# Kernel optimization log

Hardware: AMD Instinct MI355X
Metric: run time of the kernel (lower is better)

The kernel has to match this reference:

```python
import jax, jax.numpy as jnp
import numpy as np
import math

B, S, D, H = 2, 2048, 4096, 32
HD = D // H  # 128


def setup_inputs() -> dict:
    key = jax.random.key(0)
    ks = jax.random.split(key, 8)
    x = jax.random.normal(ks[0], (B, S, D), dtype=jnp.float32)
    wq = jax.random.normal(ks[1], (D, D), dtype=jnp.float32) * 0.02
    wk = jax.random.normal(ks[2], (D, D), dtype=jnp.float32) * 0.02
    wv = jax.random.normal(ks[3], (D, D), dtype=jnp.float32) * 0.02
    wo = jax.random.normal(ks[4], (D, D), dtype=jnp.float32) * 0.02
    # RoPE frequencies as in LLaMA: theta = 10000^{-2i/hd}
    inv_freq = 1.0 / (10000.0 ** (np.arange(0, HD, 2, dtype=np.float32) / HD))  # [HD/2]
    t = np.arange(S, dtype=np.float32)
    freqs = np.outer(t, inv_freq)  # [S, HD/2]
    freqs_cos = jnp.asarray(np.cos(freqs))
    freqs_sin = jnp.asarray(np.sin(freqs))
    # additive causal mask [1,1,S,S]
    neg = jnp.full((S, S), -1e9, dtype=jnp.float32)
    mask = jnp.triu(neg, k=1)[None, None, :, :]
    return {"x": x, "wq": wq, "wk": wk, "wv": wv, "wo": wo,
            "freqs_cos": freqs_cos, "freqs_sin": freqs_sin, "mask": mask}


def _apply_rope(t, cos, sin):
    # t: [b, s, h, hd]; cos/sin: [s, hd/2]. Complex mult on (even, odd) pairs.
    tr = t.reshape(*t.shape[:-1], HD // 2, 2)
    xr, xi = tr[..., 0], tr[..., 1]
    c = cos[None, :, None, :]
    s = sin[None, :, None, :]
    out_r = xr * c - xi * s
    out_i = xr * s + xi * c
    return jnp.stack([out_r, out_i], axis=-1).reshape(t.shape)


def reference(x, wq, wk, wv, wo, freqs_cos, freqs_sin, mask):
    b, s, d = x.shape
    # projections (nn.Linear: y = x @ W^T)
    xq = (x @ wq.T).reshape(b, s, H, HD)
    xk = (x @ wk.T).reshape(b, s, H, HD)
    xv = (x @ wv.T).reshape(b, s, H, HD)
    xq = _apply_rope(xq, freqs_cos, freqs_sin)
    xk = _apply_rope(xk, freqs_cos, freqs_sin)
    # [b,h,q,k] scores, softmax in fp32, then attend
    scores = jnp.einsum('bqhd,bkhd->bhqk', xq, xk) / math.sqrt(HD)
    scores = scores + mask
    probs = jax.nn.softmax(scores.astype(jnp.float32), axis=-1).astype(xq.dtype)
    out = jnp.einsum('bhqk,bkhd->bqhd', probs, xv).reshape(b, s, d)
    return out @ wo.T
```

## Files before the change

kernel.cpp:

```cpp
#include <hip/hip_runtime.h>

typedef __bf16 bf16x8 __attribute__((ext_vector_type(8)));
typedef float f32x4 __attribute__((ext_vector_type(4)));
typedef float f32x16 __attribute__((ext_vector_type(16)));
typedef unsigned short u16;
typedef unsigned int u32;
typedef u16 u16x8 __attribute__((ext_vector_type(8)));
typedef u16 u16x4 __attribute__((ext_vector_type(4)));
typedef u32 u32x4 __attribute__((ext_vector_type(4)));

#define B_ 2
#define S_ 2048
#define D_ 4096
#define H_ 32
#define HD_ 128
#define SM_SCALE 0.08838834764831845f
#define C2_ 0.12751743f

__device__ __forceinline__ u16 f2bf(float f) {
  __bf16 h = (__bf16)f;
  return __builtin_bit_cast(unsigned short, h);
}
__device__ __forceinline__ float bf2f(u16 u) {
  return (float)__builtin_bit_cast(__bf16, u);
}

#define GLD_TO_LDS16(gsrc, ldst)                                                     \
  __builtin_amdgcn_global_load_lds((__attribute__((address_space(1))) void*)(gsrc),  \
                                   (__attribute__((address_space(3))) void*)(ldst),  \
                                   16, 0, 0)

__global__ __launch_bounds__(256) void cvt5_kernel(const float* __restrict__ s0,
                                                   const float* __restrict__ s1,
                                                   const float* __restrict__ s2,
                                                   const float* __restrict__ s3,
                                                   const float* __restrict__ s4,
                                                   u16* __restrict__ d0,
                                                   u16* __restrict__ d1,
                                                   u16* __restrict__ d2,
                                                   u16* __restrict__ d3,
                                                   u16* __restrict__ d4,
                                                   int n4) {
  const int region = blockIdx.x >> 9;
  const float* src = region == 0 ? s0 : region == 1 ? s1 : region == 2 ? s2
                   : region == 3 ? s3 : s4;
  u16* dst = region == 0 ? d0 : region == 1 ? d1 : region == 2 ? d2
           : region == 3 ? d3 : d4;
  int i = (blockIdx.x & 511) * 256 + threadIdx.x;
  const int stride = 512 * 256;
  for (; i < n4; i += stride) {
    float4 v = reinterpret_cast<const float4*>(src)[i];
    u16x4 o;
    o[0] = f2bf(v.x); o[1] = f2bf(v.y); o[2] = f2bf(v.z); o[3] = f2bf(v.w);
    reinterpret_cast<u16x4*>(dst)[i] = o;
  }
}


#define LGKM0()                                            \
  do {                                                     \
    asm volatile("s_waitcnt lgkmcnt(0)" ::: "memory");     \
    __builtin_amdgcn_sched_barrier(0);                     \
  } while (0)

__device__ __forceinline__ void fill_af(bf16x8 (&dst)[4], const u16* half_base,
                                        int wr, int lane, int ks) {
#pragma unroll
  for (int m = 0; m < 4; ++m) {
    int rr = wr * 64 + m * 16 + (lane & 15);
    int c8 = (ks * 4 + (lane >> 4)) ^ (rr & 7);
    dst[m] = *reinterpret_cast<const bf16x8*>(half_base + rr * 64 + c8 * 8);
  }
}
__device__ __forceinline__ void fill_bf(bf16x8 (&dst)[2][2], const u16* half_base,
                                        int wn, int lane) {
#pragma unroll
  for (int ks = 0; ks < 2; ++ks)
#pragma unroll
    for (int n = 0; n < 2; ++n) {
      int rr = wn * 32 + n * 16 + (lane & 15);
      int c8 = (ks * 4 + (lane >> 4)) ^ (rr & 7);
      dst[ks][n] = *reinterpret_cast<const bf16x8*>(half_base + rr * 64 + c8 * 8);
    }
}

#define MFMA8(MQ, NQ, KS, AF, BF)                                                \
  do {                                                                           \
    __builtin_amdgcn_s_setprio(1);                                               \
    _Pragma("unroll") for (int m = 0; m < 4; ++m)                                \
      _Pragma("unroll") for (int n = 0; n < 2; ++n)                              \
        acc[(MQ) * 4 + m][(NQ) * 2 + n] =                                        \
            __builtin_amdgcn_mfma_f32_16x16x32_bf16(                             \
                (AF)[m], (BF)[KS][n], acc[(MQ) * 4 + m][(NQ) * 2 + n], 0, 0, 0); \
    __builtin_amdgcn_s_setprio(0);                                               \
  } while (0)

template <typename OutT, bool ROPE>
__global__ __launch_bounds__(512, 2) void gemm256_kernel(const u16* __restrict__ A,
                                                         const u16* __restrict__ Bw,
                                                         OutT* __restrict__ C,
                                                         int M, int N, int K,
                                                         const float* __restrict__ fc,
                                                         const float* __restrict__ fs) {
  __shared__ u16 As[2][2][8192];
  __shared__ u16 Bs[2][2][8192];
  const int tid = threadIdx.x;
  const int lane = tid & 63;
  const int w = tid >> 6;
  const int wr = w >> 2;
  const int wn = w & 3;
  const int nbx = N >> 8;
  const int nby = M >> 8;
  const int nwg = nby * nbx;
  int tr, tc;
  if (nby == 16 && nbx == 16) {
    int xcd = blockIdx.x & 7, j = blockIdx.x >> 3;
    tr = (xcd >> 1) * 4 + (j >> 3);
    tc = (xcd & 1) * 8 + (j & 7);
  } else {
    int wg = blockIdx.x;
    if ((nwg & 7) == 0) wg = (wg & 7) * (nwg >> 3) + (wg >> 3);
    tr = wg / nbx; tc = wg % nbx;
  }

  const size_t arow0 = (size_t)tr * 256;
  const size_t brow0 = (size_t)tc * 256;
  const int KT = K >> 6;

  auto stageA = [&](int t, int half) {
    if (t >= KT) return;
    const int k0 = t << 6;
    u16* base = &As[t & 1][half][0];
#pragma unroll
    for (int i = 0; i < 2; ++i) {
      int q = i * 512 + tid;
      int r = q >> 3;
      int c8 = (q & 7) ^ (r & 7);
      GLD_TO_LDS16(A + (arow0 + half * 128 + r) * K + k0 + c8 * 8, base + q * 8);
    }
  };
  auto stageB = [&](int t, int half) {
    if (t >= KT) return;
    const int k0 = t << 6;
    u16* base = &Bs[t & 1][half][0];
#pragma unroll
    for (int i = 0; i < 2; ++i) {
      int q = i * 512 + tid;
      int r = q >> 3;
      int c8 = (q & 7) ^ (r & 7);
      GLD_TO_LDS16(Bw + (brow0 + half * 128 + r) * K + k0 + c8 * 8, base + q * 8);
    }
  };

  f32x4 acc[8][4] = {};
  bf16x8 afX[4], afY[4], bf0[2][2], bf1[2][2];

  stageA(0, 0); stageA(0, 1); stageB(0, 0); stageB(0, 1);
  stageB(1, 0); stageB(1, 1); stageA(1, 1);
  asm volatile("s_waitcnt vmcnt(4)" ::: "memory");
  __builtin_amdgcn_s_barrier();
  __builtin_amdgcn_sched_barrier(0);
  fill_af(afX, &As[0][0][0], wr, lane, 0);
  fill_bf(bf0, &Bs[0][0][0], wn, lane);

  for (int k = 0; k < KT; ++k) {
    const int buf = k & 1, nb = buf ^ 1;
    const u16* A0 = &As[buf][0][0];
    const u16* A1 = &As[buf][1][0];
    const u16* B1L = &Bs[buf][1][0];
    const u16* A0n = &As[nb][0][0];
    const u16* B0n = &Bs[nb][0][0];

    LGKM0();
    fill_af(afY, A0, wr, lane, 1);
    fill_bf(bf1, B1L, wn, lane);
    stageA(k + 1, 0);
    MFMA8(0, 0, 0, afX, bf0);
    LGKM0();
    fill_af(afX, A1, wr, lane, 0);
    MFMA8(0, 0, 1, afY, bf0);
    __builtin_amdgcn_s_barrier();

    LGKM0();
    fill_af(afY, A1, wr, lane, 1);
    stageB(k + 2, 0);
    MFMA8(1, 0, 0, afX, bf0);
    LGKM0();
    fill_af(afX, A1, wr, lane, 0);
    MFMA8(1, 0, 1, afY, bf0);
    __builtin_amdgcn_s_barrier();

    LGKM0();
    fill_af(afY, A1, wr, lane, 1);
    stageB(k + 2, 1);
    MFMA8(1, 1, 0, afX, bf1);
    LGKM0();
    fill_af(afX, A0, wr, lane, 0);
    MFMA8(1, 1, 1, afY, bf1);
    __builtin_amdgcn_s_barrier();

    LGKM0();
    fill_af(afY, A0, wr, lane, 1);
    MFMA8(0, 1, 0, afX, bf1);
    LGKM0();
    stageA(k + 2, 1);
    if (k >= KT - 3) asm volatile("s_waitcnt vmcnt(0)" ::: "memory");
    else             asm volatile("s_waitcnt vmcnt(4)" ::: "memory");
    __builtin_amdgcn_s_barrier();
    __builtin_amdgcn_sched_barrier(0);
    if (k + 1 < KT) {
      fill_af(afX, A0n, wr, lane, 0);
      fill_bf(bf0, B0n, wn, lane);
    }
    MFMA8(0, 1, 1, afY, bf1);
    __builtin_amdgcn_s_barrier();
  }

#pragma unroll
  for (int mi = 0; mi < 8; ++mi) {
    const int mq = mi >> 2, m = mi & 3;
#pragma unroll
    for (int ni = 0; ni < 4; ++ni) {
      const int nq = ni >> 1, n = ni & 1;
#pragma unroll
      for (int r = 0; r < 4; ++r) {
        size_t row = arow0 + mq * 128 + wr * 64 + m * 16 + ((lane >> 4) << 2) + r;
        size_t col = (size_t)tc * 256 + nq * 128 + wn * 32 + n * 16 + (lane & 15);
        float v = acc[mi][ni][r];
        if constexpr (ROPE) {
          float o = __shfl_xor(v, 1);
          int s = (int)(row & (S_ - 1));
          int p = (wn * 32 + n * 16 + (lane & 14)) >> 1;
          float cv = fc[(s << 6) + p];
          float sv = fs[(s << 6) + p];
          v = (lane & 1) ? (v * cv + o * sv) : (v * cv - o * sv);
        }
        if constexpr (__is_same(OutT, float)) {
          C[row * N + col] = v;
        } else {
          C[row * N + col] = f2bf(v);
        }
      }
    }
  }
}

__global__ __launch_bounds__(512, 2) void attn_kernel(const u16* __restrict__ Q,
                                                      const u16* __restrict__ K,
                                                      const u16* __restrict__ V,
                                                      u16* __restrict__ O) {
  __shared__ u16 Ks[2][64 * 128];
  __shared__ u16 Vt[2][128 * 64];

  const int blk = blockIdx.x;
  const int pr = blk >> 6;
  const int bh = blk & 63;
  const int b = bh >> 5, h = bh & 31;
  const int tid = threadIdx.x, lane = tid & 63, w = tid >> 6;
  const int l31 = lane & 31;
  const int hi = lane >> 5;
  const int r0 = lane >> 1;
  const int dc = 2 * w + (lane & 1);
  const int vd0 = dc * 8;

  for (int ph = 0; ph < 2; ++ph) {
    const int qt = ph == 0 ? 7 - pr : pr;
    const int q0 = qt << 8;
    const int wq0 = q0 + w * 32;
    const int qg = wq0 + l31;

    bf16x8 qf[8];
#pragma unroll
    for (int kb = 0; kb < 8; ++kb)
      qf[kb] = *reinterpret_cast<const bf16x8*>(Q + (size_t)(b * S_ + qg) * D_ + h * HD_ + kb * 16 + hi * 8);

    f32x16 oacc[4] = {};
    float mrun = -__builtin_inff(), lrun = 0.f;

    const int ntiles = 4 * qt + 4;
    u16x8 vr0, vr1;

    {
#pragma unroll
      for (int it = 0; it < 2; ++it) {
        int ff = it * 512 + tid;
        int row = ff >> 4, cc = ff & 15;
        int scc = cc ^ (row & 7);
        GLD_TO_LDS16(K + (size_t)(b * S_ + row) * D_ + h * HD_ + scc * 8, &Ks[0][ff << 3]);
      }
      vr0 = *reinterpret_cast<const u16x8*>(V + (size_t)(b * S_ + 2 * r0) * D_ + h * HD_ + vd0);
      vr1 = *reinterpret_cast<const u16x8*>(V + (size_t)(b * S_ + 2 * r0 + 1) * D_ + h * HD_ + vd0);
      u32* vt32 = reinterpret_cast<u32*>(&Vt[0][0]);
#pragma unroll
      for (int j = 0; j < 8; ++j) {
        int d = vd0 + j;
        u32 val = (u32)vr0[j] | ((u32)vr1[j] << 16);
        vt32[d * 32 + ((r0 >> 2) ^ j) * 4 + (r0 & 3)] = val;
      }
    }
    __syncthreads();

    for (int t = 0; t < ntiles; ++t) {
      const int cur = t & 1, nxt = cur ^ 1;
      const bool pre = (t + 1 < ntiles);
      if (pre) {
        const int kv1 = (t + 1) << 6;
#pragma unroll
        for (int it = 0; it < 2; ++it) {
          int ff = it * 512 + tid;
          int row = ff >> 4, cc = ff & 15;
          int scc = cc ^ (row & 7);
          GLD_TO_LDS16(K + (size_t)(b * S_ + kv1 + row) * D_ + h * HD_ + scc * 8, &Ks[nxt][ff << 3]);
        }
        vr0 = *reinterpret_cast<const u16x8*>(V + (size_t)(b * S_ + kv1 + 2 * r0) * D_ + h * HD_ + vd0);
        vr1 = *reinterpret_cast<const u16x8*>(V + (size_t)(b * S_ + kv1 + 2 * r0 + 1) * D_ + h * HD_ + vd0);
      }

      const int kv0 = t << 6;
      if (kv0 <= wq0 + 31) {
        f32x16 st[2] = {};
        __builtin_amdgcn_s_setprio(1);
#pragma unroll
        for (int kvh = 0; kvh < 2; ++kvh) {
#pragma unroll
          for (int kb = 0; kb < 8; ++kb) {
            int row = kvh * 32 + l31;
            int cc = (2 * kb + hi) ^ (row & 7);
            bf16x8 kf = *reinterpret_cast<const bf16x8*>(&Ks[cur][(row << 7) + (cc << 3)]);
            st[kvh] = __builtin_amdgcn_mfma_f32_32x32x16_bf16(kf, qf[kb], st[kvh], 0, 0, 0);
          }
        }
        __builtin_amdgcn_s_setprio(0);

        if (kv0 + 63 > wq0) {
#pragma unroll
          for (int kvh = 0; kvh < 2; ++kvh)
#pragma unroll
            for (int r = 0; r < 16; ++r) {
              int kvg = kv0 + kvh * 32 + (r & 3) + 8 * (r >> 2) + 4 * hi;
              if (kvg > qg) st[kvh][r] = -1e30f;
            }
        }

        float vmax = -1e30f;
#pragma unroll
        for (int kvh = 0; kvh < 2; ++kvh)
#pragma unroll
          for (int r = 0; r < 16; ++r) vmax = fmaxf(vmax, st[kvh][r]);
        vmax = fmaxf(vmax, __shfl_xor(vmax, 32));
        if (!__all(vmax <= mrun + 64.0f)) {
          float mnew = fmaxf(mrun, vmax);
          float sc = exp2f((mrun - mnew) * C2_);
          mrun = mnew;
          lrun *= sc;
#pragma unroll
          for (int db = 0; db < 4; ++db)
#pragma unroll
            for (int r = 0; r < 16; ++r) oacc[db][r] *= sc;
        }
        float psum = 0.f;
#pragma unroll
        for (int kvh = 0; kvh < 2; ++kvh)
#pragma unroll
          for (int r = 0; r < 16; ++r) {
            float p = exp2f((st[kvh][r] - mrun) * C2_);
            st[kvh][r] = p;
            psum += p;
          }
        psum += __shfl_xor(psum, 32);
        lrun += psum;

        __builtin_amdgcn_s_setprio(1);
#pragma unroll
        for (int h2 = 0; h2 < 2; ++h2)
#pragma unroll
          for (int s2 = 0; s2 < 2; ++s2) {
            const int rb = s2 * 8;
            u32 w0, w1, w2, w3;
            asm("v_cvt_pk_bf16_f32 %0, %1, %2" : "=v"(w0) : "v"(st[h2][rb + 0]), "v"(st[h2][rb + 1]));
            asm("v_cvt_pk_bf16_f32 %0, %1, %2" : "=v"(w1) : "v"(st[h2][rb + 2]), "v"(st[h2][rb + 3]));
            asm("v_cvt_pk_bf16_f32 %0, %1, %2" : "=v"(w2) : "v"(st[h2][rb + 4]), "v"(st[h2][rb + 5]));
            asm("v_cvt_pk_bf16_f32 %0, %1, %2" : "=v"(w3) : "v"(st[h2][rb + 6]), "v"(st[h2][rb + 7]));
            u32 sw0 = (u32)__shfl_xor((int)w0, 32);
            u32 sw1 = (u32)__shfl_xor((int)w1, 32);
            u32 sw2 = (u32)__shfl_xor((int)w2, 32);
            u32 sw3 = (u32)__shfl_xor((int)w3, 32);
            u32x4 fw;
            fw[0] = hi ? sw2 : w0;
            fw[1] = hi ? sw3 : w1;
            fw[2] = hi ? w2 : sw0;
            fw[3] = hi ? w3 : sw1;
            bf16x8 pfrag = __builtin_bit_cast(bf16x8, fw);
#pragma unroll
            for (int db = 0; db < 4; ++db) {
              int d = db * 32 + l31;
              int cc = (h2 * 4 + s2 * 2 + hi) ^ (d & 7);
              bf16x8 va = *reinterpret_cast<const bf16x8*>(&Vt[cur][(d << 6) + (cc << 3)]);
              oacc[db] = __builtin_amdgcn_mfma_f32_32x32x16_bf16(va, pfrag, oacc[db], 0, 0, 0);
            }
          }
        __builtin_amdgcn_s_setprio(0);
      }

      if (pre) {
        u32* vt32 = reinterpret_cast<u32*>(&Vt[nxt][0]);
#pragma unroll
        for (int j = 0; j < 8; ++j) {
          int d = vd0 + j;
          u32 val = (u32)vr0[j] | ((u32)vr1[j] << 16);
          vt32[d * 32 + ((r0 >> 2) ^ j) * 4 + (r0 & 3)] = val;
        }
      }
      __syncthreads();
    }

    const float rinv = 1.0f / lrun;
#pragma unroll
    for (int db = 0; db < 4; ++db)
#pragma unroll
      for (int g = 0; g < 4; ++g) {
        u16x4 o4;
#pragma unroll
        for (int j = 0; j < 4; ++j) o4[j] = f2bf(oacc[db][g * 4 + j] * rinv);
        int d = db * 32 + g * 8 + 4 * hi;
        *reinterpret_cast<u16x4*>(O + (size_t)(b * S_ + qg) * D_ + h * HD_ + d) = o4;
      }
  }
}

extern "C" void kernel_launch(void* const* d_in, const int* in_sizes, int n_in,
                              void* d_out, int out_size, void* d_ws, size_t ws_size,
                              hipStream_t stream) {
  const float* x = (const float*)d_in[0];
  const float* wq = (const float*)d_in[1];
  const float* wk = (const float*)d_in[2];
  const float* wv = (const float*)d_in[3];
  const float* wo = (const float*)d_in[4];
  const float* fc = (const float*)d_in[5];
  const float* fs = (const float*)d_in[6];
  float* out = (float*)d_out;

  const size_t SLOT = (size_t)B_ * S_ * D_;
  u16* ws = (u16*)d_ws;
  u16* wqb = ws + 0 * SLOT;
  u16* wkb = ws + 1 * SLOT;
  u16* wvb = ws + 2 * SLOT;
  u16* wob = ws + 3 * SLOT;
  u16* xb  = ws + 4 * SLOT;
  u16* Qb  = ws + 5 * SLOT;
  u16* Kb  = ws + 6 * SLOT;
  u16* Vb  = ws + 7 * SLOT;
  u16* Ob  = xb;

  const int n4 = (int)(SLOT / 4);
  cvt5_kernel<<<2560, 256, 0, stream>>>(x, wq, wk, wv, wo, xb, wqb, wkb, wvb, wob, n4);

  gemm256_kernel<u16, true><<<256, 512, 0, stream>>>(xb, wqb, Qb, B_ * S_, D_, D_, fc, fs);
  gemm256_kernel<u16, true><<<256, 512, 0, stream>>>(xb, wkb, Kb, B_ * S_, D_, D_, fc, fs);
  gemm256_kernel<u16, false><<<256, 512, 0, stream>>>(xb, wvb, Vb, B_ * S_, D_, D_, fc, fs);

  attn_kernel<<<256, 512, 0, stream>>>(Qb, Kb, Vb, Ob);

  gemm256_kernel<float, false><<<256, 512, 0, stream>>>(Ob, wob, out, B_ * S_, D_, D_, fc, fs);
}
```

Measured before the change: 676.3 us.

## Fuse Q, K and V projection GEMMs into one concatenated-weight kernel launch

The three separate 256-block QKV projection GEMMs become one 768-block kernel. It treats the contiguous wq/wk/wv bf16 buffers as a single 12288-row weight matrix and routes each output tile to Q, K or V, applying RoPE only to Q and K. This removes two launch boundaries and the tail of three half-filled grids, so blocks from different projections can share the machine. The output GEMM keeps its own non-templated kernel. The fused kernel depends on the three weight slots sitting back to back in the workspace, and RoPE is now a runtime branch rather than a compile-time one.

Measured after the change: 943.3 us. +39.5%, slower.

```diff
diff --git a/kernel.cpp b/kernel.cpp
--- a/kernel.cpp
+++ b/kernel.cpp
@@ -56,7 +56,6 @@
   }
 }
 
-
 #define LGKM0()                                            \
   do {                                                     \
     asm volatile("s_waitcnt lgkmcnt(0)" ::: "memory");     \
@@ -95,11 +94,70 @@
     __builtin_amdgcn_s_setprio(0);                                               \
   } while (0)
 
-template <typename OutT, bool ROPE>
-__global__ __launch_bounds__(512, 2) void gemm256_kernel(const u16* __restrict__ A,
+#define GEMM_KLOOP_BODY()                                                        \
+  f32x4 acc[8][4] = {};                                                          \
+  bf16x8 afX[4], afY[4], bf0[2][2], bf1[2][2];                                   \
+  stageA(0, 0); stageA(0, 1); stageB(0, 0); stageB(0, 1);                        \
+  stageB(1, 0); stageB(1, 1); stageA(1, 1);                                      \
+  asm volatile("s_waitcnt vmcnt(4)" ::: "memory");                               \
+  __builtin_amdgcn_s_barrier();                                                  \
+  __builtin_amdgcn_sched_barrier(0);                                             \
+  fill_af(afX, &As[0][0][0], wr, lane, 0);                                       \
+  fill_bf(bf0, &Bs[0][0][0], wn, lane);                                          \
+  for (int k = 0; k < KT; ++k) {                                                 \
+    const int buf = k & 1, nb = buf ^ 1;                                         \
+    const u16* A0 = &As[buf][0][0];                                              \
+    const u16* A1 = &As[buf][1][0];                                              \
+    const u16* B1L = &Bs[buf][1][0];                                             \
+    const u16* A0n = &As[nb][0][0];                                              \
+    const u16* B0n = &Bs[nb][0][0];                                              \
+    LGKM0();                                                                     \
+    fill_af(afY, A0, wr, lane, 1);                                               \
+    fill_bf(bf1, B1L, wn, lane);                                                 \
+    stageA(k + 1, 0);                                                            \
+    MFMA8(0, 0, 0, afX, bf0);                                                    \
+    LGKM0();                                                                     \
+    fill_af(afX, A1, wr, lane, 0);                                               \
+    MFMA8(0, 0, 1, afY, bf0);                                                    \
+    __builtin_amdgcn_s_barrier();                                                \
+    LGKM0();                                                                     \
+    fill_af(afY, A1, wr, lane, 1);                                               \
+    stageB(k + 2, 0);                                                            \
+    MFMA8(1, 0, 0, afX, bf0);                                                    \
+    LGKM0();                                                                     \
+    fill_af(afX, A1, wr, lane, 0);                                               \
+    MFMA8(1, 0, 1, afY, bf0);                                                    \
+    __builtin_amdgcn_s_barrier();                                                \
+    LGKM0();                                                                     \
+    fill_af(afY, A1, wr, lane, 1);                                               \
+    stageB(k + 2, 1);                                                            \
+    MFMA8(1, 1, 0, afX, bf1);                                                    \
+    LGKM0();                                                                     \
+    fill_af(afX, A0, wr, lane, 0);                                               \
+    MFMA8(1, 1, 1, afY, bf1);                                                    \
+    __builtin_amdgcn_s_barrier();                                                \
+    LGKM0();                                                                     \
+    fill_af(afY, A0, wr, lane, 1);                                               \
+    MFMA8(0, 1, 0, afX, bf1);                                                    \
+    LGKM0();                                                                     \
+    stageA(k + 2, 1);                                                            \
+    if (k >= KT - 3) asm volatile("s_waitcnt vmcnt(0)" ::: "memory");            \
+    else             asm volatile("s_waitcnt vmcnt(4)" ::: "memory");            \
+    __builtin_amdgcn_s_barrier();                                                \
+    __builtin_amdgcn_sched_barrier(0);                                           \
+    if (k + 1 < KT) {                                                            \
+      fill_af(afX, A0n, wr, lane, 0);                                            \
+      fill_bf(bf0, B0n, wn, lane);                                               \
+    }                                                                            \
+    MFMA8(0, 1, 1, afY, bf1);                                                    \
+    __builtin_amdgcn_s_barrier();                                                \
+  }
+
+__global__ __launch_bounds__(512, 2) void gemmqkv_kernel(const u16* __restrict__ A,
                                                          const u16* __restrict__ Bw,
-                                                         OutT* __restrict__ C,
-                                                         int M, int N, int K,
+                                                         u16* __restrict__ Cq,
+                                                         u16* __restrict__ Ck,
+                                                         u16* __restrict__ Cv,
                                                          const float* __restrict__ fc,
                                                          const float* __restrict__ fs) {
   __shared__ u16 As[2][2][8192];
@@ -109,19 +167,10 @@
   const int w = tid >> 6;
   const int wr = w >> 2;
   const int wn = w & 3;
-  const int nbx = N >> 8;
-  const int nby = M >> 8;
-  const int nwg = nby * nbx;
-  int tr, tc;
-  if (nby == 16 && nbx == 16) {
-    int xcd = blockIdx.x & 7, j = blockIdx.x >> 3;
-    tr = (xcd >> 1) * 4 + (j >> 3);
-    tc = (xcd & 1) * 8 + (j & 7);
-  } else {
-    int wg = blockIdx.x;
-    if ((nwg & 7) == 0) wg = (wg & 7) * (nwg >> 3) + (wg >> 3);
-    tr = wg / nbx; tc = wg % nbx;
-  }
+  const int K = D_;
+  const int nbx = 48;
+  int wg = (blockIdx.x & 7) * 96 + (blockIdx.x >> 3);
+  const int tr = wg / nbx, tc = wg % nbx;
 
   const size_t arow0 = (size_t)tr * 256;
   const size_t brow0 = (size_t)tc * 256;
@@ -152,70 +201,12 @@
     }
   };
 
-  f32x4 acc[8][4] = {};
-  bf16x8 afX[4], afY[4], bf0[2][2], bf1[2][2];
-
-  stageA(0, 0); stageA(0, 1); stageB(0, 0); stageB(0, 1);
-  stageB(1, 0); stageB(1, 1); stageA(1, 1);
-  asm volatile("s_waitcnt vmcnt(4)" ::: "memory");
-  __builtin_amdgcn_s_barrier();
-  __builtin_amdgcn_sched_barrier(0);
-  fill_af(afX, &As[0][0][0], wr, lane, 0);
-  fill_bf(bf0, &Bs[0][0][0], wn, lane);
-
-  for (int k = 0; k < KT; ++k) {
-    const int buf = k & 1, nb = buf ^ 1;
-    const u16* A0 = &As[buf][0][0];
-    const u16* A1 = &As[buf][1][0];
-    const u16* B1L = &Bs[buf][1][0];
-    const u16* A0n = &As[nb][0][0];
-    const u16* B0n = &Bs[nb][0][0];
-
-    LGKM0();
-    fill_af(afY, A0, wr, lane, 1);
-    fill_bf(bf1, B1L, wn, lane);
-    stageA(k + 1, 0);
-    MFMA8(0, 0, 0, afX, bf0);
-    LGKM0();
-    fill_af(afX, A1, wr, lane, 0);
-    MFMA8(0, 0, 1, afY, bf0);
-    __builtin_amdgcn_s_barrier();
-
-    LGKM0();
-    fill_af(afY, A1, wr, lane, 1);
-    stageB(k + 2, 0);
-    MFMA8(1, 0, 0, afX, bf0);
-    LGKM0();
-    fill_af(afX, A1, wr, lane, 0);
-    MFMA8(1, 0, 1, afY, bf0);
-    __builtin_amdgcn_s_barrier();
-
-    LGKM0();
-    fill_af(afY, A1, wr, lane, 1);
-    stageB(k + 2, 1);
-    MFMA8(1, 1, 0, afX, bf1);
-    LGKM0();
-    fill_af(afX, A0, wr, lane, 0);
-    MFMA8(1, 1, 1, afY, bf1);
-    __builtin_amdgcn_s_barrier();
-
-    LGKM0();
-    fill_af(afY, A0, wr, lane, 1);
-    MFMA8(0, 1, 0, afX, bf1);
-    LGKM0();
-    stageA(k + 2, 1);
-    if (k >= KT - 3) asm volatile("s_waitcnt vmcnt(0)" ::: "memory");
-    else             asm volatile("s_waitcnt vmcnt(4)" ::: "memory");
-    __builtin_amdgcn_s_barrier();
-    __builtin_amdgcn_sched_barrier(0);
-    if (k + 1 < KT) {
-      fill_af(afX, A0n, wr, lane, 0);
-      fill_bf(bf0, B0n, wn, lane);
-    }
-    MFMA8(0, 1, 1, afY, bf1);
-    __builtin_amdgcn_s_barrier();
-  }
-
+  GEMM_KLOOP_BODY();
+
+  const int proj = tc >> 4;
+  u16* Cb = proj == 0 ? Cq : proj == 1 ? Ck : Cv;
+  const int tcl = tc & 15;
+  const bool rope = (proj < 2);
 #pragma unroll
   for (int mi = 0; mi < 8; ++mi) {
     const int mq = mi >> 2, m = mi & 3;
@@ -225,21 +216,80 @@
 #pragma unroll
       for (int r = 0; r < 4; ++r) {
         size_t row = arow0 + mq * 128 + wr * 64 + m * 16 + ((lane >> 4) << 2) + r;
-        size_t col = (size_t)tc * 256 + nq * 128 + wn * 32 + n * 16 + (lane & 15);
+        size_t col = (size_t)tcl * 256 + nq * 128 + wn * 32 + n * 16 + (lane & 15);
         float v = acc[mi][ni][r];
-        if constexpr (ROPE) {
-          float o = __shfl_xor(v, 1);
+        float o = __shfl_xor(v, 1);
+        if (rope) {
           int s = (int)(row & (S_ - 1));
           int p = (wn * 32 + n * 16 + (lane & 14)) >> 1;
           float cv = fc[(s << 6) + p];
           float sv = fs[(s << 6) + p];
           v = (lane & 1) ? (v * cv + o * sv) : (v * cv - o * sv);
         }
-        if constexpr (__is_same(OutT, float)) {
-          C[row * N + col] = v;
-        } else {
-          C[row * N + col] = f2bf(v);
-        }
+        Cb[row * D_ + col] = f2bf(v);
+      }
+    }
+  }
+}
+
+__global__ __launch_bounds__(512, 2) void gemm256_kernel(const u16* __restrict__ A,
+                                                         const u16* __restrict__ Bw,
+                                                         float* __restrict__ C,
+                                                         int M, int N, int K) {
+  __shared__ u16 As[2][2][8192];
+  __shared__ u16 Bs[2][2][8192];
+  const int tid = threadIdx.x;
+  const int lane = tid & 63;
+  const int w = tid >> 6;
+  const int wr = w >> 2;
+  const int wn = w & 3;
+  const int nbx = N >> 8;
+  int xcd = blockIdx.x & 7, j = blockIdx.x >> 3;
+  const int tr = (xcd >> 1) * 4 + (j >> 3);
+  const int tc = (xcd & 1) * 8 + (j & 7);
+
+  const size_t arow0 = (size_t)tr * 256;
+  const size_t brow0 = (size_t)tc * 256;
+  const int KT = K >> 6;
+
+  auto stageA = [&](int t, int half) {
+    if (t >= KT) return;
+    const int k0 = t << 6;
+    u16* base = &As[t & 1][half][0];
+#pragma unroll
+    for (int i = 0; i < 2; ++i) {
+      int q = i * 512 + tid;
+      int r = q >> 3;
+      int c8 = (q & 7) ^ (r & 7);
+      GLD_TO_LDS16(A + (arow0 + half * 128 + r) * K + k0 + c8 * 8, base + q * 8);
+    }
+  };
+  auto stageB = [&](int t, int half) {
+    if (t >= KT) return;
+    const int k0 = t << 6;
+    u16* base = &Bs[t & 1][half][0];
+#pragma unroll
+    for (int i = 0; i < 2; ++i) {
+      int q = i * 512 + tid;
+      int r = q >> 3;
+      int c8 = (q & 7) ^ (r & 7);
+      GLD_TO_LDS16(Bw + (brow0 + half * 128 + r) * K + k0 + c8 * 8, base + q * 8);
+    }
+  };
+
+  GEMM_KLOOP_BODY();
+
+#pragma unroll
+  for (int mi = 0; mi < 8; ++mi) {
+    const int mq = mi >> 2, m = mi & 3;
+#pragma unroll
+    for (int ni = 0; ni < 4; ++ni) {
+      const int nq = ni >> 1, n = ni & 1;
+#pragma unroll
+      for (int r = 0; r < 4; ++r) {
+        size_t row = arow0 + mq * 128 + wr * 64 + m * 16 + ((lane >> 4) << 2) + r;
+        size_t col = (size_t)tc * 256 + nq * 128 + wn * 32 + n * 16 + (lane & 15);
+        C[row * N + col] = acc[mi][ni][r];
       }
     }
   }
@@ -455,11 +505,9 @@
   const int n4 = (int)(SLOT / 4);
   cvt5_kernel<<<2560, 256, 0, stream>>>(x, wq, wk, wv, wo, xb, wqb, wkb, wvb, wob, n4);
 
-  gemm256_kernel<u16, true><<<256, 512, 0, stream>>>(xb, wqb, Qb, B_ * S_, D_, D_, fc, fs);
-  gemm256_kernel<u16, true><<<256, 512, 0, stream>>>(xb, wkb, Kb, B_ * S_, D_, D_, fc, fs);
-  gemm256_kernel<u16, false><<<256, 512, 0, stream>>>(xb, wvb, Vb, B_ * S_, D_, D_, fc, fs);
+  gemmqkv_kernel<<<768, 512, 0, stream>>>(xb, wqb, Qb, Kb, Vb, fc, fs);
 
   attn_kernel<<<256, 512, 0, stream>>>(Qb, Kb, Vb, Ob);
 
-  gemm256_kernel<float, false><<<256, 512, 0, stream>>>(Ob, wob, out, B_ * S_, D_, D_, fc, fs);
-}
+  gemm256_kernel<<<256, 512, 0, stream>>>(Ob, wob, out, B_ * S_, D_, D_);
+}
```

## Reorder GEMM k-loop by k-substep to reuse A/B fragments across quadrants

Applied to the files above, without the earlier changes.

The inner loop now walks all four output quadrants for the first k-substep, then all four for the second, instead of walking quadrants in the outer order. B fragments are loaded per substep into two small register sets, and each A fragment now feeds two quadrants before it is replaced. This roughly halves the LDS fragment reads per iteration and drops one workgroup barrier. The cost is a more intricate interleaving of LDS loads, waits and buffer-overwrite ordering, which must stay correct with respect to the async global-to-LDS staging.

Result: no change. 688.9 us (+1.9%).

```diff
diff --git a/kernel.cpp b/kernel.cpp
--- a/kernel.cpp
+++ b/kernel.cpp
@@ -63,8 +63,8 @@
     __builtin_amdgcn_sched_barrier(0);                     \
   } while (0)
 
-__device__ __forceinline__ void fill_af(bf16x8 (&dst)[4], const u16* half_base,
-                                        int wr, int lane, int ks) {
+__device__ __forceinline__ void fill_a(bf16x8 (&dst)[4], const u16* half_base,
+                                       int wr, int lane, int ks) {
 #pragma unroll
   for (int m = 0; m < 4; ++m) {
     int rr = wr * 64 + m * 16 + (lane & 15);
@@ -72,26 +72,24 @@
     dst[m] = *reinterpret_cast<const bf16x8*>(half_base + rr * 64 + c8 * 8);
   }
 }
-__device__ __forceinline__ void fill_bf(bf16x8 (&dst)[2][2], const u16* half_base,
-                                        int wn, int lane) {
-#pragma unroll
-  for (int ks = 0; ks < 2; ++ks)
-#pragma unroll
-    for (int n = 0; n < 2; ++n) {
-      int rr = wn * 32 + n * 16 + (lane & 15);
-      int c8 = (ks * 4 + (lane >> 4)) ^ (rr & 7);
-      dst[ks][n] = *reinterpret_cast<const bf16x8*>(half_base + rr * 64 + c8 * 8);
-    }
-}
-
-#define MFMA8(MQ, NQ, KS, AF, BF)                                                \
+__device__ __forceinline__ void fill_b2(bf16x8 (&dst)[2], const u16* half_base,
+                                        int wn, int lane, int ks) {
+#pragma unroll
+  for (int n = 0; n < 2; ++n) {
+    int rr = wn * 32 + n * 16 + (lane & 15);
+    int c8 = (ks * 4 + (lane >> 4)) ^ (rr & 7);
+    dst[n] = *reinterpret_cast<const bf16x8*>(half_base + rr * 64 + c8 * 8);
+  }
+}
+
+#define MFMA8Q(MQ, NQ, A4, B2)                                                   \
   do {                                                                           \
     __builtin_amdgcn_s_setprio(1);                                               \
     _Pragma("unroll") for (int m = 0; m < 4; ++m)                                \
       _Pragma("unroll") for (int n = 0; n < 2; ++n)                              \
         acc[(MQ) * 4 + m][(NQ) * 2 + n] =                                        \
             __builtin_amdgcn_mfma_f32_16x16x32_bf16(                             \
-                (AF)[m], (BF)[KS][n], acc[(MQ) * 4 + m][(NQ) * 2 + n], 0, 0, 0); \
+                (A4)[m], (B2)[n], acc[(MQ) * 4 + m][(NQ) * 2 + n], 0, 0, 0);     \
     __builtin_amdgcn_s_setprio(0);                                               \
   } while (0)
 
@@ -153,66 +151,59 @@
   };
 
   f32x4 acc[8][4] = {};
-  bf16x8 afX[4], afY[4], bf0[2][2], bf1[2][2];
+  bf16x8 aX[4], aY[4], bX[2], bY[2];
 
   stageA(0, 0); stageA(0, 1); stageB(0, 0); stageB(0, 1);
   stageB(1, 0); stageB(1, 1); stageA(1, 1);
   asm volatile("s_waitcnt vmcnt(4)" ::: "memory");
   __builtin_amdgcn_s_barrier();
   __builtin_amdgcn_sched_barrier(0);
-  fill_af(afX, &As[0][0][0], wr, lane, 0);
-  fill_bf(bf0, &Bs[0][0][0], wn, lane);
+  fill_a(aX, &As[0][0][0], wr, lane, 0);
+  fill_b2(bX, &Bs[0][0][0], wn, lane, 0);
 
   for (int k = 0; k < KT; ++k) {
     const int buf = k & 1, nb = buf ^ 1;
     const u16* A0 = &As[buf][0][0];
     const u16* A1 = &As[buf][1][0];
+    const u16* B0L = &Bs[buf][0][0];
     const u16* B1L = &Bs[buf][1][0];
     const u16* A0n = &As[nb][0][0];
     const u16* B0n = &Bs[nb][0][0];
 
     LGKM0();
-    fill_af(afY, A0, wr, lane, 1);
-    fill_bf(bf1, B1L, wn, lane);
+    fill_b2(bY, B1L, wn, lane, 0);
     stageA(k + 1, 0);
-    MFMA8(0, 0, 0, afX, bf0);
-    LGKM0();
-    fill_af(afX, A1, wr, lane, 0);
-    MFMA8(0, 0, 1, afY, bf0);
+    MFMA8Q(0, 0, aX, bX);
+    LGKM0();
+    fill_a(aY, A1, wr, lane, 0);
+    MFMA8Q(0, 1, aX, bY);
+    LGKM0();
+    MFMA8Q(1, 1, aY, bY);
+    fill_a(aX, A1, wr, lane, 1);
+    fill_b2(bY, B0L, wn, lane, 1);
+    MFMA8Q(1, 0, aY, bX);
+    LGKM0();
+    fill_b2(bX, B1L, wn, lane, 1);
+    MFMA8Q(1, 0, aX, bY);
     __builtin_amdgcn_s_barrier();
-
-    LGKM0();
-    fill_af(afY, A1, wr, lane, 1);
+    LGKM0();
+    fill_a(aY, A0, wr, lane, 1);
     stageB(k + 2, 0);
-    MFMA8(1, 0, 0, afX, bf0);
-    LGKM0();
-    fill_af(afX, A1, wr, lane, 0);
-    MFMA8(1, 0, 1, afY, bf0);
+    MFMA8Q(1, 1, aX, bX);
     __builtin_amdgcn_s_barrier();
-
-    LGKM0();
-    fill_af(afY, A1, wr, lane, 1);
+    LGKM0();
     stageB(k + 2, 1);
-    MFMA8(1, 1, 0, afX, bf1);
-    LGKM0();
-    fill_af(afX, A0, wr, lane, 0);
-    MFMA8(1, 1, 1, afY, bf1);
-    __builtin_amdgcn_s_barrier();
-
-    LGKM0();
-    fill_af(afY, A0, wr, lane, 1);
-    MFMA8(0, 1, 0, afX, bf1);
-    LGKM0();
     stageA(k + 2, 1);
+    MFMA8Q(0, 1, aY, bX);
     if (k >= KT - 3) asm volatile("s_waitcnt vmcnt(0)" ::: "memory");
     else             asm volatile("s_waitcnt vmcnt(4)" ::: "memory");
     __builtin_amdgcn_s_barrier();
     __builtin_amdgcn_sched_barrier(0);
     if (k + 1 < KT) {
-      fill_af(afX, A0n, wr, lane, 0);
-      fill_bf(bf0, B0n, wn, lane);
-    }
-    MFMA8(0, 1, 1, afY, bf1);
+      fill_a(aX, A0n, wr, lane, 0);
+      fill_b2(bX, B0n, wn, lane, 0);
+    }
+    MFMA8Q(0, 0, aY, bY);
     __builtin_amdgcn_s_barrier();
   }
 
```

## Restructure GEMM main loop into four quadrant phases with full-K fragment loads

Applied to the files above, without the earlier changes.

Replaces the eight half-K MFMA groups per K-tile, with their interleaved A/B fragment ping-pong, by four quadrant phases. Each phase loads both K-halves of the fragments and then issues sixteen MFMAs, and the prefetch order of global-to-LDS stages changes to match. The goal is fewer LDS wait points and simpler scheduling per tile, at the cost of less overlap between fragment reads and MFMA work and more barriers per iteration. The prologue stage order and the vmcnt thresholds are changed as well, so correctness depends on the new stage ordering matching the waits.

Measured after the change: 669.6 us, median of 2. About the same (-1.0%).

```diff
diff --git a/kernel.cpp b/kernel.cpp
--- a/kernel.cpp
+++ b/kernel.cpp
@@ -63,16 +63,18 @@
     __builtin_amdgcn_sched_barrier(0);                     \
   } while (0)
 
-__device__ __forceinline__ void fill_af(bf16x8 (&dst)[4], const u16* half_base,
-                                        int wr, int lane, int ks) {
-#pragma unroll
-  for (int m = 0; m < 4; ++m) {
-    int rr = wr * 64 + m * 16 + (lane & 15);
-    int c8 = (ks * 4 + (lane >> 4)) ^ (rr & 7);
-    dst[m] = *reinterpret_cast<const bf16x8*>(half_base + rr * 64 + c8 * 8);
-  }
-}
-__device__ __forceinline__ void fill_bf(bf16x8 (&dst)[2][2], const u16* half_base,
+__device__ __forceinline__ void fill_aq(bf16x8 (&dst)[2][4], const u16* half_base,
+                                        int wr, int lane) {
+#pragma unroll
+  for (int ks = 0; ks < 2; ++ks)
+#pragma unroll
+    for (int m = 0; m < 4; ++m) {
+      int rr = wr * 64 + m * 16 + (lane & 15);
+      int c8 = (ks * 4 + (lane >> 4)) ^ (rr & 7);
+      dst[ks][m] = *reinterpret_cast<const bf16x8*>(half_base + rr * 64 + c8 * 8);
+    }
+}
+__device__ __forceinline__ void fill_bq(bf16x8 (&dst)[2][2], const u16* half_base,
                                         int wn, int lane) {
 #pragma unroll
   for (int ks = 0; ks < 2; ++ks)
@@ -84,14 +86,16 @@
     }
 }
 
-#define MFMA8(MQ, NQ, KS, AF, BF)                                                \
+#define MFMA16(MQ, NQ, AF, BF)                                                   \
   do {                                                                           \
     __builtin_amdgcn_s_setprio(1);                                               \
-    _Pragma("unroll") for (int m = 0; m < 4; ++m)                                \
-      _Pragma("unroll") for (int n = 0; n < 2; ++n)                              \
-        acc[(MQ) * 4 + m][(NQ) * 2 + n] =                                        \
-            __builtin_amdgcn_mfma_f32_16x16x32_bf16(                             \
-                (AF)[m], (BF)[KS][n], acc[(MQ) * 4 + m][(NQ) * 2 + n], 0, 0, 0); \
+    _Pragma("unroll") for (int ks = 0; ks < 2; ++ks)                             \
+      _Pragma("unroll") for (int m = 0; m < 4; ++m)                              \
+        _Pragma("unroll") for (int n = 0; n < 2; ++n)                            \
+          acc[(MQ) * 4 + m][(NQ) * 2 + n] =                                      \
+              __builtin_amdgcn_mfma_f32_16x16x32_bf16(                           \
+                  (AF)[ks][m], (BF)[ks][n], acc[(MQ) * 4 + m][(NQ) * 2 + n],     \
+                  0, 0, 0);                                                      \
     __builtin_amdgcn_s_setprio(0);                                               \
   } while (0)
 
@@ -153,66 +157,49 @@
   };
 
   f32x4 acc[8][4] = {};
-  bf16x8 afX[4], afY[4], bf0[2][2], bf1[2][2];
-
-  stageA(0, 0); stageA(0, 1); stageB(0, 0); stageB(0, 1);
-  stageB(1, 0); stageB(1, 1); stageA(1, 1);
+  bf16x8 aF[2][4], bF0[2][2], bF1[2][2];
+
+  stageA(0, 0); stageB(0, 0); stageA(0, 1); stageB(0, 1);
+  stageA(1, 0); stageB(1, 0);
   asm volatile("s_waitcnt vmcnt(4)" ::: "memory");
   __builtin_amdgcn_s_barrier();
   __builtin_amdgcn_sched_barrier(0);
-  fill_af(afX, &As[0][0][0], wr, lane, 0);
-  fill_bf(bf0, &Bs[0][0][0], wn, lane);
-
-  for (int k = 0; k < KT; ++k) {
-    const int buf = k & 1, nb = buf ^ 1;
-    const u16* A0 = &As[buf][0][0];
-    const u16* A1 = &As[buf][1][0];
-    const u16* B1L = &Bs[buf][1][0];
-    const u16* A0n = &As[nb][0][0];
-    const u16* B0n = &Bs[nb][0][0];
-
+
+  for (int t = 0; t < KT; ++t) {
+    const int buf = t & 1;
+    const u16* Ah0 = &As[buf][0][0];
+    const u16* Ah1 = &As[buf][1][0];
+    const u16* Bh0 = &Bs[buf][0][0];
+    const u16* Bh1 = &Bs[buf][1][0];
+
+    fill_aq(aF, Ah0, wr, lane);
+    fill_bq(bF0, Bh0, wn, lane);
+    stageA(t + 1, 1);
+    __builtin_amdgcn_s_barrier();
     LGKM0();
-    fill_af(afY, A0, wr, lane, 1);
-    fill_bf(bf1, B1L, wn, lane);
-    stageA(k + 1, 0);
-    MFMA8(0, 0, 0, afX, bf0);
+    MFMA16(0, 0, aF, bF0);
+    __builtin_amdgcn_s_barrier();
+
+    fill_bq(bF1, Bh1, wn, lane);
+    stageB(t + 1, 1);
+    __builtin_amdgcn_s_barrier();
     LGKM0();
-    fill_af(afX, A1, wr, lane, 0);
-    MFMA8(0, 0, 1, afY, bf0);
-    __builtin_amdgcn_s_barrier();
-
+    MFMA16(0, 1, aF, bF1);
+    __builtin_amdgcn_s_barrier();
+
+    fill_aq(aF, Ah1, wr, lane);
+    stageA(t + 2, 0);
+    __builtin_amdgcn_s_barrier();
     LGKM0();
-    fill_af(afY, A1, wr, lane, 1);
-    stageB(k + 2, 0);
-    MFMA8(1, 0, 0, afX, bf0);
-    LGKM0();
-    fill_af(afX, A1, wr, lane, 0);
-    MFMA8(1, 0, 1, afY, bf0);
-    __builtin_amdgcn_s_barrier();
-
-    LGKM0();
-    fill_af(afY, A1, wr, lane, 1);
-    stageB(k + 2, 1);
-    MFMA8(1, 1, 0, afX, bf1);
-    LGKM0();
-    fill_af(afX, A0, wr, lane, 0);
-    MFMA8(1, 1, 1, afY, bf1);
-    __builtin_amdgcn_s_barrier();
-
-    LGKM0();
-    fill_af(afY, A0, wr, lane, 1);
-    MFMA8(0, 1, 0, afX, bf1);
-    LGKM0();
-    stageA(k + 2, 1);
-    if (k >= KT - 3) asm volatile("s_waitcnt vmcnt(0)" ::: "memory");
+    MFMA16(1, 0, aF, bF0);
+    __builtin_amdgcn_s_barrier();
+
+    stageB(t + 2, 0);
+    if (t >= KT - 2) asm volatile("s_waitcnt vmcnt(0)" ::: "memory");
     else             asm volatile("s_waitcnt vmcnt(4)" ::: "memory");
     __builtin_amdgcn_s_barrier();
     __builtin_amdgcn_sched_barrier(0);
-    if (k + 1 < KT) {
-      fill_af(afX, A0n, wr, lane, 0);
-      fill_bf(bf0, B0n, wn, lane);
-    }
-    MFMA8(0, 1, 1, afY, bf1);
+    MFMA16(1, 1, aF, bF1);
     __builtin_amdgcn_s_barrier();
   }
 
```
